# Kernel optimization log

Hardware: AMD Instinct MI355X
Metric: run time of the kernel (lower is better)

## Reference

```python
import jax, jax.numpy as jnp
import numpy as np

B = 131072
T = 101

def _glorot(k, fan_in, fan_out):
    lim = (6.0 / (fan_in + fan_out)) ** 0.5
    return jax.random.uniform(k, (fan_in, fan_out), minval=-lim, maxval=lim, dtype=jnp.float32)

def setup_inputs() -> dict:
    key = jax.random.key(0)
    ks = jax.random.split(key, 8)
    y0 = jax.random.uniform(ks[0], (B, 3), dtype=jnp.float32)
    y0 = y0 / jnp.sum(y0, axis=-1, keepdims=True)  # SIR fractions
    t_span = jnp.arange(T, dtype=jnp.float32) * 2.0  # matches step_size=2.0 grid
    beta = jax.random.uniform(ks[1], (B,), dtype=jnp.float32)
    gamma = jax.random.uniform(ks[2], (B,), dtype=jnp.float32)
    W1 = _glorot(ks[3], 5, 64);   b1 = jnp.zeros((64,), jnp.float32)
    W2 = _glorot(ks[4], 64, 128); b2 = jnp.zeros((128,), jnp.float32)
    W3 = _glorot(ks[5], 128, 64); b3 = jnp.zeros((64,), jnp.float32)
    W4 = _glorot(ks[6], 64, 3);   b4 = jnp.zeros((3,), jnp.float32)
    return {"y0": y0, "t_span": t_span, "beta": beta, "gamma": gamma,
            "W1": W1, "b1": b1, "W2": W2, "b2": b2,
            "W3": W3, "b3": b3, "W4": W4, "b4": b4}

def reference(y0, t_span, beta, gamma, W1, b1, W2, b2, W3, b3, W4, b4):
    # augmented state y = [S, I, R, beta, gamma], shape [B, 5]
    y0_aug = jnp.concatenate([y0, beta[:, None], gamma[:, None]], axis=1)

    def f(y):  # derivative function; t is unused by the net
        h = jnp.tanh(y @ W1 + b1)
        h = jnp.tanh(h @ W2 + b2)
        h = jnp.tanh(h @ W3 + b3)
        d = h @ W4 + b4  # [B, 3]
        return jnp.concatenate([d, jnp.zeros_like(y[:, :2])], axis=1)  # beta/gamma constant

    dts = t_span[1:] - t_span[:-1]  # each interval == one RK4 step (step_size=2.0)

    def step(y, dt):
        k1 = f(y)
        k2 = f(y + 0.5 * dt * k1)
        k3 = f(y + 0.5 * dt * k2)
        k4 = f(y + dt * k3)
        y_next = y + (dt / 6.0) * (k1 + 2.0 * k2 + 2.0 * k3 + k4)
        return y_next, y_next

    _, ys = jax.lax.scan(step, y0_aug, dts)          # [T-1, B, 5]
    sol = jnp.concatenate([y0_aug[None], ys], axis=0)  # [T, B, 5]
    return jax.nn.softmax(sol[:, :, :3], axis=-1)    # [T, B, 3]
```

## Files before the change

kernel.cpp:

```cpp
#include <hip/hip_runtime.h>


#define NW1  (5 * 64)
#define NB1  64
#define NW2  (64 * 128)
#define NB2  128
#define NW3  (128 * 64)
#define NB3  64
#define NW4  (64 * 3)
#define NB4  3

#define oW1T 0
#define oB1  (oW1T + NW1)
#define oW2  (oB1 + NB1)
#define oB2  (oW2 + NW2)
#define oW3  (oB2 + NB2)
#define oB3  (oW3 + NW3)
#define oW4  (oB3 + NB3)
#define oB4  (oW4 + NW4)
#define NTOT (oB4 + NB4)

__device__ __forceinline__ void store_softmax(float* __restrict__ out, size_t base,
                                              float a, float b, float c) {
    float m  = fmaxf(a, fmaxf(b, c));
    float e0 = expf(a - m);
    float e1 = expf(b - m);
    float e2 = expf(c - m);
    float s  = e0 + e1 + e2;
    out[base + 0] = e0 / s;
    out[base + 1] = e1 / s;
    out[base + 2] = e2 / s;
}

__global__ __launch_bounds__(128, 2) void sir_rk4_kernel(
    const float* __restrict__ y0,   const float* __restrict__ tspan,
    const float* __restrict__ beta, const float* __restrict__ gamma,
    const double* __restrict__ P,
    float* __restrict__ out, int B, int T)
{
    __shared__ float hbuf[64][128];

    const int tid = threadIdx.x;
    const int b = blockIdx.x * 128 + tid;
    if (b >= B) return;

    const double* W1T = P + oW1T;
    const double* B1v = P + oB1;
    const double* W2  = P + oW2;
    const double* B2v = P + oB2;
    const double* W3  = P + oW3;
    const double* B3v = P + oB3;
    const double* W4  = P + oW4;
    const double* B4v = P + oB4;

    double ys = (double)y0[b * 3 + 0];
    double yi = (double)y0[b * 3 + 1];
    double yr = (double)y0[b * 3 + 2];
    const double be = (double)beta[b];
    const double ga = (double)gamma[b];

    store_softmax(out, (size_t)b * 3, (float)ys, (float)yi, (float)yr);

    #pragma unroll 1
    for (int t = 0; t < T - 1; ++t) {
        double dt = (double)tspan[t + 1] - (double)tspan[t];

        double ks0 = 0.0, ks1 = 0.0, ks2 = 0.0;
        double zs = ys, zi = yi, zr = yr;

        #pragma unroll 1
        for (int st = 0; st < 4; ++st) {
            #pragma unroll 2
            for (int j = 0; j < 64; ++j) {
                const double* w = W1T + j * 5;
                double ta = fma(w[0], zs, B1v[j]);
                double tb = w[2] * zr;
                ta = fma(w[1], zi, ta);
                tb = fma(w[3], be, tb);
                ta = fma(w[4], ga, ta);
                hbuf[j][tid] = tanhf((float)(ta + tb));
            }

            double acc3[64];
            #pragma unroll
            for (int j = 0; j < 64; ++j) acc3[j] = B3v[j];

            #pragma unroll 1
            for (int c = 0; c < 8; ++c) {
                double h2[16];
                #pragma unroll
                for (int k = 0; k < 16; ++k) h2[k] = B2v[c * 16 + k];

                #pragma unroll 4
                for (int i = 0; i < 64; ++i) {
                    double hv = (double)hbuf[i][tid];
                    const double* w = W2 + i * 128 + c * 16;
                    #pragma unroll
                    for (int k = 0; k < 16; ++k)
                        h2[k] = fma(w[k], hv, h2[k]);
                }

                #pragma unroll
                for (int k = 0; k < 16; ++k)
                    h2[k] = (double)tanhf((float)h2[k]);

                #pragma unroll
                for (int k = 0; k < 16; ++k) {
                    const double* w3 = W3 + (size_t)(c * 16 + k) * 64;
                    #pragma unroll
                    for (int j = 0; j < 64; ++j)
                        acc3[j] = fma(w3[j], h2[k], acc3[j]);
                }
            }

            #pragma unroll
            for (int j = 0; j < 64; ++j) hbuf[j][tid] = (float)acc3[j];

            double e0 = B4v[0], e1 = B4v[1], e2 = B4v[2];
            #pragma unroll 2
            for (int j = 0; j < 64; ++j) {
                double h = (double)tanhf(hbuf[j][tid]);
                const double* w4 = W4 + j * 3;
                e0 = fma(w4[0], h, e0);
                e1 = fma(w4[1], h, e1);
                e2 = fma(w4[2], h, e2);
            }

            double w = (st == 1 || st == 2) ? 2.0 : 1.0;
            ks0 = fma(w, e0, ks0);
            ks1 = fma(w, e1, ks1);
            ks2 = fma(w, e2, ks2);
            double a = (st < 2) ? 0.5 * dt : dt;
            zs = fma(a, e0, ys);
            zi = fma(a, e1, yi);
            zr = fma(a, e2, yr);
        }

        double c6 = dt * (1.0 / 6.0);
        ys = fma(c6, ks0, ys);
        yi = fma(c6, ks1, yi);
        yr = fma(c6, ks2, yr);

        store_softmax(out, ((size_t)(t + 1) * B + b) * 3, (float)ys, (float)yi, (float)yr);
    }
}

__global__ void stage_params_kernel(
    const float* __restrict__ W1, const float* __restrict__ b1,
    const float* __restrict__ W2, const float* __restrict__ b2,
    const float* __restrict__ W3, const float* __restrict__ b3,
    const float* __restrict__ W4, const float* __restrict__ b4,
    double* __restrict__ P)
{
    int idx = blockIdx.x * blockDim.x + threadIdx.x;
    if (idx >= NTOT) return;
    float v;
    if (idx < oB1)       { int u = idx - oW1T; int j = u / 5; int q = u % 5; v = W1[q * 64 + j]; }
    else if (idx < oW2)  v = b1[idx - oB1];
    else if (idx < oB2)  v = W2[idx - oW2];
    else if (idx < oW3)  v = b2[idx - oB2];
    else if (idx < oB3)  v = W3[idx - oW3];
    else if (idx < oW4)  v = b3[idx - oB3];
    else if (idx < oB4)  v = W4[idx - oW4];
    else                 v = b4[idx - oB4];
    P[idx] = (double)v;
}

extern "C" void kernel_launch(void* const* d_in, const int* in_sizes, int n_in,
                              void* d_out, int out_size, void* d_ws, size_t ws_size,
                              hipStream_t stream) {
    const float* y0    = (const float*)d_in[0];
    const float* tspan = (const float*)d_in[1];
    const float* beta  = (const float*)d_in[2];
    const float* gamma = (const float*)d_in[3];
    const float* W1    = (const float*)d_in[4];
    const float* b1    = (const float*)d_in[5];
    const float* W2    = (const float*)d_in[6];
    const float* b2    = (const float*)d_in[7];
    const float* W3    = (const float*)d_in[8];
    const float* b3    = (const float*)d_in[9];
    const float* W4    = (const float*)d_in[10];
    const float* b4    = (const float*)d_in[11];

    int B = in_sizes[0] / 3;
    int T = in_sizes[1];
    float* out = (float*)d_out;

    double* P = (double*)d_ws;
    stage_params_kernel<<<(NTOT + 255) / 256, 256, 0, stream>>>(
        W1, b1, W2, b2, W3, b3, W4, b4, P);

    int blocks = (B + 127) / 128;
    sir_rk4_kernel<<<blocks, 128, 0, stream>>>(
        y0, tspan, beta, gamma, P, out, B, T);
}
```

Baseline: 90.81 ms.

## Stage W2/W3 as float and software-pipeline weight loads in FP64 MLP

W2 and W3 are now staged in float precision instead of double, which halves the bytes of the scalar weight loads in the two big layers. The layer-2 loop is restructured into 16 chunks of 8 outputs, with a rotating set of register buffers that prefetch weight rows two steps ahead. The layer-3 accumulation uses a triple-buffered 16-wide prefetch. Arithmetic stays in FP64, so the gain depends on whether load latency was limiting throughput rather than FP64 FMA rate. The extra buffers add register pressure.

```diff
diff --git a/kernel.cpp b/kernel.cpp
--- a/kernel.cpp
+++ b/kernel.cpp
@@ -1,24 +1,17 @@
 #include <hip/hip_runtime.h>
 
 
-#define NW1  (5 * 64)
-#define NB1  64
-#define NW2  (64 * 128)
-#define NB2  128
-#define NW3  (128 * 64)
-#define NB3  64
-#define NW4  (64 * 3)
-#define NB4  3
-
-#define oW1T 0
-#define oB1  (oW1T + NW1)
-#define oW2  (oB1 + NB1)
-#define oB2  (oW2 + NW2)
-#define oW3  (oB2 + NB2)
-#define oB3  (oW3 + NW3)
-#define oW4  (oB3 + NB3)
-#define oB4  (oW4 + NW4)
-#define NTOT (oB4 + NB4)
+#define NDBL 771
+#define dW1T 0
+#define dB1  320
+#define dB2  384
+#define dB3  512
+#define dW4  576
+#define dB4  768
+#define NFLT 16384
+#define fW2  0
+#define fW3  8192
+#define NTOT (NDBL + NFLT)
 
 __device__ __forceinline__ void store_softmax(float* __restrict__ out, size_t base,
                                               float a, float b, float c) {
@@ -35,7 +28,7 @@
 __global__ __launch_bounds__(128, 2) void sir_rk4_kernel(
     const float* __restrict__ y0,   const float* __restrict__ tspan,
     const float* __restrict__ beta, const float* __restrict__ gamma,
-    const double* __restrict__ P,
+    const double* __restrict__ PD,  const float* __restrict__ PF,
     float* __restrict__ out, int B, int T)
 {
     __shared__ float hbuf[64][128];
@@ -44,14 +37,14 @@
     const int b = blockIdx.x * 128 + tid;
     if (b >= B) return;
 
-    const double* W1T = P + oW1T;
-    const double* B1v = P + oB1;
-    const double* W2  = P + oW2;
-    const double* B2v = P + oB2;
-    const double* W3  = P + oW3;
-    const double* B3v = P + oB3;
-    const double* W4  = P + oW4;
-    const double* B4v = P + oB4;
+    const double* W1T = PD + dW1T;
+    const double* B1v = PD + dB1;
+    const double* B2v = PD + dB2;
+    const double* B3v = PD + dB3;
+    const double* W4v = PD + dW4;
+    const double* B4v = PD + dB4;
+    const float*  W2f = PF + fW2;
+    const float*  W3f = PF + fW3;
 
     double ys = (double)y0[b * 3 + 0];
     double yi = (double)y0[b * 3 + 1];
@@ -86,30 +79,73 @@
             for (int j = 0; j < 64; ++j) acc3[j] = B3v[j];
 
             #pragma unroll 1
-            for (int c = 0; c < 8; ++c) {
-                double h2[16];
-                #pragma unroll
-                for (int k = 0; k < 16; ++k) h2[k] = B2v[c * 16 + k];
-
-                #pragma unroll 4
-                for (int i = 0; i < 64; ++i) {
-                    double hv = (double)hbuf[i][tid];
-                    const double* w = W2 + i * 128 + c * 16;
-                    #pragma unroll
-                    for (int k = 0; k < 16; ++k)
-                        h2[k] = fma(w[k], hv, h2[k]);
+            for (int c = 0; c < 16; ++c) {
+                double h2[8];
+                #pragma unroll
+                for (int k = 0; k < 8; ++k) h2[k] = B2v[c * 8 + k];
+
+                const float* wt = W2f + c * 8;
+
+                float wb0[8], wb1[8], wb2[8], wb3[8];
+                #pragma unroll
+                for (int q = 0; q < 8; ++q) wb0[q] = wt[0 * 128 + q];
+                #pragma unroll
+                for (int q = 0; q < 8; ++q) wb1[q] = wt[1 * 128 + q];
+
+                #pragma unroll 1
+                for (int i = 0; i < 64; i += 4) {
+                    #pragma unroll
+                    for (int q = 0; q < 8; ++q) wb2[q] = wt[(i + 2) * 128 + q];
+                    {
+                        double hv = (double)hbuf[i][tid];
+                        #pragma unroll
+                        for (int q = 0; q < 8; ++q) h2[q] = fma((double)wb0[q], hv, h2[q]);
+                    }
+                    #pragma unroll
+                    for (int q = 0; q < 8; ++q) wb3[q] = wt[(i + 3) * 128 + q];
+                    {
+                        double hv = (double)hbuf[i + 1][tid];
+                        #pragma unroll
+                        for (int q = 0; q < 8; ++q) h2[q] = fma((double)wb1[q], hv, h2[q]);
+                    }
+                    #pragma unroll
+                    for (int q = 0; q < 8; ++q) wb0[q] = wt[(i + 4) * 128 + q];
+                    {
+                        double hv = (double)hbuf[i + 2][tid];
+                        #pragma unroll
+                        for (int q = 0; q < 8; ++q) h2[q] = fma((double)wb2[q], hv, h2[q]);
+                    }
+                    #pragma unroll
+                    for (int q = 0; q < 8; ++q) wb1[q] = wt[(i + 5) * 128 + q];
+                    {
+                        double hv = (double)hbuf[i + 3][tid];
+                        #pragma unroll
+                        for (int q = 0; q < 8; ++q) h2[q] = fma((double)wb3[q], hv, h2[q]);
+                    }
                 }
 
-                #pragma unroll
-                for (int k = 0; k < 16; ++k)
-                    h2[k] = (double)tanhf((float)h2[k]);
-
-                #pragma unroll
-                for (int k = 0; k < 16; ++k) {
-                    const double* w3 = W3 + (size_t)(c * 16 + k) * 64;
-                    #pragma unroll
-                    for (int j = 0; j < 64; ++j)
-                        acc3[j] = fma(w3[j], h2[k], acc3[j]);
+                const float* w3t = W3f + c * 512;
+                float ub[3][16];
+                #pragma unroll
+                for (int q = 0; q < 16; ++q) ub[0][q] = w3t[q];
+                #pragma unroll
+                for (int q = 0; q < 16; ++q) ub[1][q] = w3t[16 + q];
+
+                #pragma unroll
+                for (int kk = 0; kk < 8; ++kk) {
+                    double h = (double)tanhf((float)h2[kk]);
+                    #pragma unroll
+                    for (int q4 = 0; q4 < 4; ++q4) {
+                        const int p = kk * 4 + q4;
+                        if (p + 2 < 32) {
+                            #pragma unroll
+                            for (int q = 0; q < 16; ++q)
+                                ub[(p + 2) % 3][q] = w3t[(p + 2) * 16 + q];
+                        }
+                        #pragma unroll
+                        for (int j = 0; j < 16; ++j)
+                            acc3[q4 * 16 + j] = fma((double)ub[p % 3][j], h, acc3[q4 * 16 + j]);
+                    }
                 }
             }
 
@@ -120,7 +156,7 @@
             #pragma unroll 2
             for (int j = 0; j < 64; ++j) {
                 double h = (double)tanhf(hbuf[j][tid]);
-                const double* w4 = W4 + j * 3;
+                const double* w4 = W4v + j * 3;
                 e0 = fma(w4[0], h, e0);
                 e1 = fma(w4[1], h, e1);
                 e2 = fma(w4[2], h, e2);
@@ -150,20 +186,23 @@
     const float* __restrict__ W2, const float* __restrict__ b2,
     const float* __restrict__ W3, const float* __restrict__ b3,
     const float* __restrict__ W4, const float* __restrict__ b4,
-    double* __restrict__ P)
+    double* __restrict__ PD, float* __restrict__ PF)
 {
     int idx = blockIdx.x * blockDim.x + threadIdx.x;
     if (idx >= NTOT) return;
-    float v;
-    if (idx < oB1)       { int u = idx - oW1T; int j = u / 5; int q = u % 5; v = W1[q * 64 + j]; }
-    else if (idx < oW2)  v = b1[idx - oB1];
-    else if (idx < oB2)  v = W2[idx - oW2];
-    else if (idx < oW3)  v = b2[idx - oB2];
-    else if (idx < oB3)  v = W3[idx - oW3];
-    else if (idx < oW4)  v = b3[idx - oB3];
-    else if (idx < oB4)  v = W4[idx - oW4];
-    else                 v = b4[idx - oB4];
-    P[idx] = (double)v;
+    if (idx < NDBL) {
+        float v;
+        if (idx < dB1)      { int u = idx - dW1T; int j = u / 5; int q = u % 5; v = W1[q * 64 + j]; }
+        else if (idx < dB2) v = b1[idx - dB1];
+        else if (idx < dB3) v = b2[idx - dB2];
+        else if (idx < dW4) v = b3[idx - dB3];
+        else if (idx < dB4) v = W4[idx - dW4];
+        else                v = b4[idx - dB4];
+        PD[idx] = (double)v;
+    } else {
+        int f = idx - NDBL;
+        PF[f] = (f < fW3) ? W2[f] : W3[f - fW3];
+    }
 }
 
 extern "C" void kernel_launch(void* const* d_in, const int* in_sizes, int n_in,
@@ -186,11 +225,13 @@
     int T = in_sizes[1];
     float* out = (float*)d_out;
 
-    double* P = (double*)d_ws;
+    double* PD = (double*)d_ws;
+    float*  PF = (float*)((char*)d_ws + (size_t)NDBL * sizeof(double));
+
     stage_params_kernel<<<(NTOT + 255) / 256, 256, 0, stream>>>(
-        W1, b1, W2, b2, W3, b3, W4, b4, P);
+        W1, b1, W2, b2, W3, b3, W4, b4, PD, PF);
 
     int blocks = (B + 127) / 128;
     sir_rk4_kernel<<<blocks, 128, 0, stream>>>(
-        y0, tspan, beta, gamma, P, out, B, T);
-}
+        y0, tspan, beta, gamma, PD, PF, out, B, T);
+}
```

New measurement: 109.5 ms. +20.6%, slower.
